# Performance work log

Measured on AMD Instinct MI355X. Metric: run time of the kernel, lower is better.

The kernel has to match this reference:

```python
import jax, jax.numpy as jnp
import numpy as np

N_NODES = 50000
N_EDGES = 800000
D_IN = 128
D_HID = 512
D_OUT = 128


def setup_inputs() -> dict:
    key = jax.random.key(0)
    k1, k2, k3, k4, k5, k6 = jax.random.split(key, 6)
    input_matrix = jax.random.normal(k1, (N_NODES, D_IN), dtype=jnp.float32)
    adjacency_coo_matrix = jax.random.randint(k2, (2, N_EDGES), 0, N_NODES, dtype=jnp.int64)
    # fc net params (torch Linear: y = x @ W.T + b); store W already transposed [D_IN, D_HID]
    lim_fc = 1.0 / np.sqrt(D_IN)
    fc_w = jax.random.uniform(k3, (D_IN, D_HID), dtype=jnp.float32, minval=-lim_fc, maxval=lim_fc)
    fc_b = jax.random.uniform(k4, (D_HID,), dtype=jnp.float32, minval=-lim_fc, maxval=lim_fc)
    # xavier_uniform for [D_IN + D_HID, D_OUT]
    lim_w = np.sqrt(6.0 / (D_IN + D_HID + D_OUT))
    weights_matrix = jax.random.uniform(k5, (D_IN + D_HID, D_OUT), dtype=jnp.float32, minval=-lim_w, maxval=lim_w)
    return {
        "input_matrix": input_matrix,
        "fc_w": fc_w,
        "fc_b": fc_b,
        "weights_matrix": weights_matrix,
        "adjacency_coo_matrix": adjacency_coo_matrix,
    }


def reference(input_matrix, fc_w, fc_b, weights_matrix, adjacency_coo_matrix):
    edge_src, edge_trg = adjacency_coo_matrix[0], adjacency_coo_matrix[1]
    n_nodes = input_matrix.shape[0]
    # gather neighbor features: [E, D_IN]
    neighbors = input_matrix[edge_trg]
    # per-edge MLP + relu: [E, D_HID]
    neighbors_repr = jax.nn.relu(neighbors @ fc_w + fc_b)
    # scatter-max reduce into per-node slots; relu outputs are >= 0, and
    # empty segments map to 0 (matching torch_scatter zero-fill), so clamp at 0
    agg = jax.ops.segment_max(neighbors_repr, edge_src, num_segments=n_nodes)
    agg = jnp.maximum(agg, 0.0)
    concat = jnp.concatenate([input_matrix, agg], axis=1)  # [N, D_IN + D_HID]
    return concat @ weights_matrix  # [N, D_OUT]
```

## Files before the change

kernel.cpp:

```cpp
#include <hip/hip_runtime.h>
#include <hip/hip_bf16.h>

#define N_NODES 50000
#define N_EDGES 800000
#define D_IN 128
#define D_HID 512
#define D_OUT 128
#define CAT_DIM 640
#define CAP 64

typedef __attribute__((ext_vector_type(8))) short short8;
typedef __attribute__((ext_vector_type(4))) float floatx4;

__device__ __forceinline__ unsigned short f2bf(float f) {
    unsigned u = __float_as_uint(f);
    unsigned r = u + 0x7fffu + ((u >> 16) & 1u);
    return (unsigned short)(r >> 16);
}


#define PREP_CASTX_BLOCKS   6250
#define PREP_FCW_BLOCKS      256
#define PREP_W2_BLOCKS       320
#define PREP_DEG_BLOCKS      196
#define PREP_TOTAL_BLOCKS  (PREP_CASTX_BLOCKS + PREP_FCW_BLOCKS + PREP_W2_BLOCKS + PREP_DEG_BLOCKS + 1)

__global__ void prep_kernel(const float* __restrict__ X, const float* __restrict__ fcW,
                            const float* __restrict__ Wm, const int* __restrict__ adj,
                            unsigned short* __restrict__ concat,
                            unsigned short* __restrict__ fcwT,
                            unsigned short* __restrict__ WT,
                            int* __restrict__ deg, int* __restrict__ flag) {
    int b = blockIdx.x;
    int tid = threadIdx.x;
    if (b < PREP_CASTX_BLOCKS) {
        int t = b * 256 + tid;
        int row = t >> 5;
        int cg2 = (t & 31) * 4;
        float4 v = *(const float4*)(X + (size_t)row * D_IN + cg2);
        unsigned short o[4] = { f2bf(v.x), f2bf(v.y), f2bf(v.z), f2bf(v.w) };
        *(unsigned long long*)(concat + (size_t)row * CAT_DIM + cg2) = *(unsigned long long*)o;
        return;
    }
    b -= PREP_CASTX_BLOCKS;
    if (b < PREP_FCW_BLOCKS) {
        int idx = b * 256 + tid;
        int k = idx >> 9;
        int n = idx & (D_HID - 1);
        fcwT[n * D_IN + k] = f2bf(fcW[idx]);
        return;
    }
    b -= PREP_FCW_BLOCKS;
    if (b < PREP_W2_BLOCKS) {
        int idx = b * 256 + tid;
        int k = idx >> 7;
        int n = idx & (D_OUT - 1);
        WT[n * CAT_DIM + k] = f2bf(Wm[idx]);
        return;
    }
    b -= PREP_W2_BLOCKS;
    if (b < PREP_DEG_BLOCKS) {
        int idx = b * 256 + tid;
        if (idx < N_NODES) deg[idx] = 0;
        return;
    }
    if (tid < 64) {
        int v = adj[2 * tid + 1];
        unsigned long long m = __ballot(v != 0);
        if (tid == 0) *flag = (m == 0ULL) ? 2 : 1;
    }
}


__device__ __forceinline__ void hist_edges(const int* __restrict__ adj, int s, int e0,
                                           int* __restrict__ deg, int* __restrict__ edge_list) {
    int src0, src1, trg0, trg1;
    if (s == 2) {
        int4 vs = *(const int4*)(adj + 2 * (size_t)e0);
        int4 vt = *(const int4*)(adj + 2 * ((size_t)N_EDGES + e0));
        src0 = vs.x; src1 = vs.z;
        trg0 = vt.x; trg1 = vt.z;
    } else {
        int2 vs = *(const int2*)(adj + e0);
        int2 vt = *(const int2*)(adj + N_EDGES + e0);
        src0 = vs.x; src1 = vs.y;
        trg0 = vt.x; trg1 = vt.y;
    }
    int p0 = atomicAdd(&deg[src0], 1);
    if (p0 < CAP) edge_list[src0 * CAP + p0] = trg0;
    int p1 = atomicAdd(&deg[src1], 1);
    if (p1 < CAP) edge_list[src1 * CAP + p1] = trg1;
}


#define GPAD 8
#define SM64_BYTES ((64 + 128) * (64 + GPAD) * 2)

template<int BIAS_RELU, int OUT_BF16>
__device__ __forceinline__ void gemm_tile64(char* smem,
    const unsigned short* __restrict__ A, int lda,
    const unsigned short* __restrict__ Bt, int ldb,
    const float* __restrict__ bias, void* __restrict__ Cout, int ldc,
    int M, int K, int bm, int bn)
{
    constexpr int BK = 64;
    typedef unsigned short Row[BK + GPAD];
    Row* As = (Row*)smem;
    Row* Bs = (Row*)(smem + 64 * (BK + GPAD) * 2);
    int tid = threadIdx.x;
    int lane = tid & 63, w = tid >> 6;
    int wm = (w >> 1) * 32, wn = (w & 1) * 64;
    int q = lane >> 4, l16 = lane & 15;
    floatx4 acc[2][4] = {};
    int ra = tid >> 2;
    int ca = (tid & 3) * 8;
    int rb = tid >> 1;
    int cb = (tid & 1) * 8;

    for (int k0 = 0; k0 < K; k0 += BK) {
        {
            int gr = bm + ra;
            const unsigned short* ap = A + (size_t)gr * lda + k0 + ca;
            #pragma unroll
            for (int p = 0; p < 2; ++p) {
                uint4 va = make_uint4(0u, 0u, 0u, 0u);
                if (gr < M) va = *(const uint4*)(ap + p * 32);
                *(uint4*)(&As[ra][ca + p * 32]) = va;
            }
        }
        {
            const unsigned short* bp = Bt + (size_t)(bn + rb) * ldb + k0 + cb;
            #pragma unroll
            for (int p = 0; p < 4; ++p)
                *(uint4*)(&Bs[rb][cb + p * 16]) = *(const uint4*)(bp + p * 16);
        }
        __syncthreads();
        #pragma unroll
        for (int ks = 0; ks < 2; ++ks) {
            short8 af[2], bf[4];
            #pragma unroll
            for (int mi = 0; mi < 2; ++mi)
                af[mi] = *(const short8*)(&As[wm + mi * 16 + l16][ks * 32 + q * 8]);
            #pragma unroll
            for (int ni = 0; ni < 4; ++ni)
                bf[ni] = *(const short8*)(&Bs[wn + ni * 16 + l16][ks * 32 + q * 8]);
            #pragma unroll
            for (int mi = 0; mi < 2; ++mi)
                #pragma unroll
                for (int ni = 0; ni < 4; ++ni)
                    acc[mi][ni] = __builtin_amdgcn_mfma_f32_16x16x32_bf16(af[mi], bf[ni], acc[mi][ni], 0, 0, 0);
        }
        __syncthreads();
    }

    #pragma unroll
    for (int mi = 0; mi < 2; ++mi) {
        #pragma unroll
        for (int ni = 0; ni < 4; ++ni) {
            #pragma unroll
            for (int r = 0; r < 4; ++r) {
                int row = bm + wm + mi * 16 + q * 4 + r;
                int col = bn + wn + ni * 16 + l16;
                if (row < M) {
                    float v = acc[mi][ni][r];
                    if (BIAS_RELU) v = fmaxf(v + bias[col], 0.0f);
                    if (OUT_BF16) ((unsigned short*)Cout)[(size_t)row * ldc + col] = f2bf(v);
                    else          ((float*)Cout)[(size_t)row * ldc + col] = v;
                }
            }
        }
    }
}


#define HIST_VB     1563
#define GEMM1_MT     782
#define GEMM1_TILES (GEMM1_MT * 4)

__global__ __launch_bounds__(256)
void mid_kernel(const int* __restrict__ adj, const int* __restrict__ flag,
                int* __restrict__ deg, int* __restrict__ edge_list,
                const unsigned short* __restrict__ concat,
                const unsigned short* __restrict__ fcwT,
                const float* __restrict__ fcb,
                unsigned short* __restrict__ F) {
    if (blockIdx.x < HIST_VB) {
        int e0 = (blockIdx.x * 256 + threadIdx.x) * 2;
        if (e0 < N_EDGES) hist_edges(adj, flag[0], e0, deg, edge_list);
        return;
    }
    __shared__ char smem[SM64_BYTES];
    int tile = blockIdx.x - HIST_VB;
    gemm_tile64<1, 1>(smem, concat, CAT_DIM, fcwT, D_IN, fcb, F, D_HID,
                      N_NODES, D_IN, (tile >> 2) * 64, (tile & 3) * 128);
}


__device__ __forceinline__ void fmax_bf16x8(float* acc, const uint4& p) {
    const unsigned* a = (const unsigned*)&p;
    #pragma unroll
    for (int j = 0; j < 4; ++j) {
        unsigned u = a[j];
        acc[2 * j]     = fmaxf(acc[2 * j],     __uint_as_float(u << 16));
        acc[2 * j + 1] = fmaxf(acc[2 * j + 1], __uint_as_float(u & 0xffff0000u));
    }
}

__global__ __launch_bounds__(256)
void aggregate_kernel(const unsigned short* __restrict__ F,
                      const int* __restrict__ deg,
                      const int* __restrict__ edge_list,
                      unsigned short* __restrict__ concat) {
    int gw = (blockIdx.x * 256 + threadIdx.x) >> 6;
    if (gw >= N_NODES) return;
    int lane = threadIdx.x & 63;
    int d = deg[gw];
    d = d < CAP ? d : CAP;
    const int* el = edge_list + gw * CAP;
    float acc[8] = {0.f, 0.f, 0.f, 0.f, 0.f, 0.f, 0.f, 0.f};
    int i = 0;
    for (; i + 2 <= d; i += 2) {
        int t0 = el[i], t1 = el[i + 1];
        uint4 p0 = *(const uint4*)(F + (size_t)t0 * D_HID + lane * 8);
        uint4 p1 = *(const uint4*)(F + (size_t)t1 * D_HID + lane * 8);
        fmax_bf16x8(acc, p0);
        fmax_bf16x8(acc, p1);
    }
    if (i < d) {
        uint4 p0 = *(const uint4*)(F + (size_t)el[i] * D_HID + lane * 8);
        fmax_bf16x8(acc, p0);
    }
    unsigned out[4];
    #pragma unroll
    for (int j = 0; j < 4; ++j) {
        unsigned lo = __float_as_uint(acc[2 * j]) >> 16;
        unsigned hi = __float_as_uint(acc[2 * j + 1]) & 0xffff0000u;
        out[j] = lo | hi;
    }
    *(uint4*)(concat + (size_t)gw * CAT_DIM + D_IN + lane * 8) = *(uint4*)out;
}


__global__ __launch_bounds__(256)
void gemm2_kernel(const unsigned short* __restrict__ concat,
                  const unsigned short* __restrict__ WT,
                  float* __restrict__ out) {
    __shared__ char smem[SM64_BYTES];
    gemm_tile64<0, 0>(smem, concat, CAT_DIM, WT, CAT_DIM, nullptr, out, D_OUT,
                      N_NODES, CAT_DIM, blockIdx.x * 64, 0);
}


extern "C" void kernel_launch(void* const* d_in, const int* in_sizes, int n_in,
                              void* d_out, int out_size, void* d_ws, size_t ws_size,
                              hipStream_t stream) {
    const float* X    = (const float*)d_in[0];
    const float* fc_w = (const float*)d_in[1];
    const float* fc_b = (const float*)d_in[2];
    const float* Wm   = (const float*)d_in[3];
    const int*   adj  = (const int*)d_in[4];
    float* outp = (float*)d_out;

    char* ws = (char*)d_ws;
    size_t off = 0;
    auto alloc = [&](size_t bytes) -> void* {
        void* p = ws + off;
        off = (off + bytes + 255) & ~(size_t)255;
        return p;
    };
    unsigned short* concat = (unsigned short*)alloc((size_t)N_NODES * CAT_DIM * 2);
    unsigned short* F      = (unsigned short*)alloc((size_t)N_NODES * D_HID * 2);
    unsigned short* fcwT   = (unsigned short*)alloc((size_t)D_HID * D_IN * 2);
    unsigned short* WT     = (unsigned short*)alloc((size_t)D_OUT * CAT_DIM * 2);
    int* deg       = (int*)alloc((size_t)N_NODES * 4);
    int* edge_list = (int*)alloc((size_t)N_NODES * CAP * 4);
    int* flag      = (int*)alloc(256);

    prep_kernel<<<PREP_TOTAL_BLOCKS, 256, 0, stream>>>(X, fc_w, Wm, adj, concat, fcwT, WT, deg, flag);
    mid_kernel<<<HIST_VB + GEMM1_TILES, 256, 0, stream>>>(adj, flag, deg, edge_list,
                                                          concat, fcwT, fc_b, F);
    aggregate_kernel<<<(N_NODES * 64) / 256, 256, 0, stream>>>(F, deg, edge_list, concat);
    gemm2_kernel<<<GEMM1_MT, 256, 0, stream>>>(concat, WT, outp);
}
```

Baseline: 288.9 us.

## Fuse scatter-max aggregation with the output GEMM, dropping the concat buffer

Merges the aggregation and second GEMM into one kernel. Each block aggregates 32 nodes into shared memory, then runs the output GEMM from shared memory plus a compact bf16 copy of X. The concat buffer and its global write and reread go away, along with one launch. B-operand fragments now load straight from global with no LDS staging, aggregation unrolls by 4, and the smaller 32-row tiles with serial per-wave node loops may reduce parallelism.

```diff
diff --git a/kernel.cpp b/kernel.cpp
--- a/kernel.cpp
+++ b/kernel.cpp
@@ -27,19 +27,17 @@
 
 __global__ void prep_kernel(const float* __restrict__ X, const float* __restrict__ fcW,
                             const float* __restrict__ Wm, const int* __restrict__ adj,
-                            unsigned short* __restrict__ concat,
+                            unsigned short* __restrict__ Xb,
                             unsigned short* __restrict__ fcwT,
                             unsigned short* __restrict__ WT,
                             int* __restrict__ deg, int* __restrict__ flag) {
     int b = blockIdx.x;
     int tid = threadIdx.x;
     if (b < PREP_CASTX_BLOCKS) {
-        int t = b * 256 + tid;
-        int row = t >> 5;
-        int cg2 = (t & 31) * 4;
-        float4 v = *(const float4*)(X + (size_t)row * D_IN + cg2);
+        size_t base = ((size_t)b * 256 + tid) * 4;
+        float4 v = *(const float4*)(X + base);
         unsigned short o[4] = { f2bf(v.x), f2bf(v.y), f2bf(v.z), f2bf(v.w) };
-        *(unsigned long long*)(concat + (size_t)row * CAT_DIM + cg2) = *(unsigned long long*)o;
+        *(unsigned long long*)(Xb + base) = *(unsigned long long*)o;
         return;
     }
     b -= PREP_CASTX_BLOCKS;
@@ -96,12 +94,11 @@
 #define GPAD 8
 #define SM64_BYTES ((64 + 128) * (64 + GPAD) * 2)
 
-template<int BIAS_RELU, int OUT_BF16>
-__device__ __forceinline__ void gemm_tile64(char* smem,
-    const unsigned short* __restrict__ A, int lda,
-    const unsigned short* __restrict__ Bt, int ldb,
-    const float* __restrict__ bias, void* __restrict__ Cout, int ldc,
-    int M, int K, int bm, int bn)
+__device__ __forceinline__ void gemm1_tile(char* smem,
+    const unsigned short* __restrict__ A,
+    const unsigned short* __restrict__ Bt,
+    const float* __restrict__ bias,
+    unsigned short* __restrict__ F, int bm, int bn)
 {
     constexpr int BK = 64;
     typedef unsigned short Row[BK + GPAD];
@@ -117,19 +114,19 @@
     int rb = tid >> 1;
     int cb = (tid & 1) * 8;
 
-    for (int k0 = 0; k0 < K; k0 += BK) {
+    for (int k0 = 0; k0 < D_IN; k0 += BK) {
         {
             int gr = bm + ra;
-            const unsigned short* ap = A + (size_t)gr * lda + k0 + ca;
+            const unsigned short* ap = A + (size_t)gr * D_IN + k0 + ca;
             #pragma unroll
             for (int p = 0; p < 2; ++p) {
                 uint4 va = make_uint4(0u, 0u, 0u, 0u);
-                if (gr < M) va = *(const uint4*)(ap + p * 32);
+                if (gr < N_NODES) va = *(const uint4*)(ap + p * 32);
                 *(uint4*)(&As[ra][ca + p * 32]) = va;
             }
         }
         {
-            const unsigned short* bp = Bt + (size_t)(bn + rb) * ldb + k0 + cb;
+            const unsigned short* bp = Bt + (size_t)(bn + rb) * D_IN + k0 + cb;
             #pragma unroll
             for (int p = 0; p < 4; ++p)
                 *(uint4*)(&Bs[rb][cb + p * 16]) = *(const uint4*)(bp + p * 16);
@@ -161,11 +158,9 @@
             for (int r = 0; r < 4; ++r) {
                 int row = bm + wm + mi * 16 + q * 4 + r;
                 int col = bn + wn + ni * 16 + l16;
-                if (row < M) {
-                    float v = acc[mi][ni][r];
-                    if (BIAS_RELU) v = fmaxf(v + bias[col], 0.0f);
-                    if (OUT_BF16) ((unsigned short*)Cout)[(size_t)row * ldc + col] = f2bf(v);
-                    else          ((float*)Cout)[(size_t)row * ldc + col] = v;
+                if (row < N_NODES) {
+                    float v = fmaxf(acc[mi][ni][r] + bias[col], 0.0f);
+                    F[(size_t)row * D_HID + col] = f2bf(v);
                 }
             }
         }
@@ -180,7 +175,7 @@
 __global__ __launch_bounds__(256)
 void mid_kernel(const int* __restrict__ adj, const int* __restrict__ flag,
                 int* __restrict__ deg, int* __restrict__ edge_list,
-                const unsigned short* __restrict__ concat,
+                const unsigned short* __restrict__ Xb,
                 const unsigned short* __restrict__ fcwT,
                 const float* __restrict__ fcb,
                 unsigned short* __restrict__ F) {
@@ -191,10 +186,13 @@
     }
     __shared__ char smem[SM64_BYTES];
     int tile = blockIdx.x - HIST_VB;
-    gemm_tile64<1, 1>(smem, concat, CAT_DIM, fcwT, D_IN, fcb, F, D_HID,
-                      N_NODES, D_IN, (tile >> 2) * 64, (tile & 3) * 128);
-}
-
+    gemm1_tile(smem, Xb, fcwT, fcb, F, (tile >> 2) * 64, (tile & 3) * 128);
+}
+
+
+#define AG_BM     32
+#define AG_BLOCKS 1563
+#define APAD      8
 
 __device__ __forceinline__ void fmax_bf16x8(float* acc, const uint4& p) {
     const unsigned* a = (const unsigned*)&p;
@@ -207,47 +205,86 @@
 }
 
 __global__ __launch_bounds__(256)
-void aggregate_kernel(const unsigned short* __restrict__ F,
-                      const int* __restrict__ deg,
-                      const int* __restrict__ edge_list,
-                      unsigned short* __restrict__ concat) {
-    int gw = (blockIdx.x * 256 + threadIdx.x) >> 6;
-    if (gw >= N_NODES) return;
-    int lane = threadIdx.x & 63;
-    int d = deg[gw];
-    d = d < CAP ? d : CAP;
-    const int* el = edge_list + gw * CAP;
-    float acc[8] = {0.f, 0.f, 0.f, 0.f, 0.f, 0.f, 0.f, 0.f};
-    int i = 0;
-    for (; i + 2 <= d; i += 2) {
-        int t0 = el[i], t1 = el[i + 1];
-        uint4 p0 = *(const uint4*)(F + (size_t)t0 * D_HID + lane * 8);
-        uint4 p1 = *(const uint4*)(F + (size_t)t1 * D_HID + lane * 8);
-        fmax_bf16x8(acc, p0);
-        fmax_bf16x8(acc, p1);
-    }
-    if (i < d) {
-        uint4 p0 = *(const uint4*)(F + (size_t)el[i] * D_HID + lane * 8);
-        fmax_bf16x8(acc, p0);
-    }
-    unsigned out[4];
-    #pragma unroll
-    for (int j = 0; j < 4; ++j) {
-        unsigned lo = __float_as_uint(acc[2 * j]) >> 16;
-        unsigned hi = __float_as_uint(acc[2 * j + 1]) & 0xffff0000u;
-        out[j] = lo | hi;
-    }
-    *(uint4*)(concat + (size_t)gw * CAT_DIM + D_IN + lane * 8) = *(uint4*)out;
-}
-
-
-__global__ __launch_bounds__(256)
-void gemm2_kernel(const unsigned short* __restrict__ concat,
-                  const unsigned short* __restrict__ WT,
-                  float* __restrict__ out) {
-    __shared__ char smem[SM64_BYTES];
-    gemm_tile64<0, 0>(smem, concat, CAT_DIM, WT, CAT_DIM, nullptr, out, D_OUT,
-                      N_NODES, CAT_DIM, blockIdx.x * 64, 0);
+void aggemm_kernel(const unsigned short* __restrict__ F,
+                   const int* __restrict__ deg,
+                   const int* __restrict__ edge_list,
+                   const unsigned short* __restrict__ Xb,
+                   const unsigned short* __restrict__ WT,
+                   float* __restrict__ out) {
+    __shared__ unsigned short aggS[AG_BM][D_HID + APAD];
+    int tid = threadIdx.x;
+    int lane = tid & 63, wv = tid >> 6;
+    int bm = blockIdx.x * AG_BM;
+
+    for (int nn = 0; nn < 8; ++nn) {
+        int lr = wv * 8 + nn;
+        int node = bm + lr;
+        if (node < N_NODES) {
+            int d = deg[node];
+            d = d < CAP ? d : CAP;
+            const int* el = edge_list + node * CAP;
+            float acc[8] = {0.f, 0.f, 0.f, 0.f, 0.f, 0.f, 0.f, 0.f};
+            int i = 0;
+            for (; i + 4 <= d; i += 4) {
+                uint4 p0 = *(const uint4*)(F + (size_t)el[i]     * D_HID + lane * 8);
+                uint4 p1 = *(const uint4*)(F + (size_t)el[i + 1] * D_HID + lane * 8);
+                uint4 p2 = *(const uint4*)(F + (size_t)el[i + 2] * D_HID + lane * 8);
+                uint4 p3 = *(const uint4*)(F + (size_t)el[i + 3] * D_HID + lane * 8);
+                fmax_bf16x8(acc, p0);
+                fmax_bf16x8(acc, p1);
+                fmax_bf16x8(acc, p2);
+                fmax_bf16x8(acc, p3);
+            }
+            for (; i < d; ++i) {
+                uint4 p0 = *(const uint4*)(F + (size_t)el[i] * D_HID + lane * 8);
+                fmax_bf16x8(acc, p0);
+            }
+            unsigned o[4];
+            #pragma unroll
+            for (int j = 0; j < 4; ++j) {
+                unsigned lo = __float_as_uint(acc[2 * j]) >> 16;
+                unsigned hi = __float_as_uint(acc[2 * j + 1]) & 0xffff0000u;
+                o[j] = lo | hi;
+            }
+            *(uint4*)(&aggS[lr][lane * 8]) = *(uint4*)o;
+        }
+    }
+    __syncthreads();
+
+    int wm = (wv >> 1) * 16, wn = (wv & 1) * 64;
+    int q = lane >> 4, l16 = lane & 15;
+    floatx4 acc[4] = {};
+    int arow = bm + wm + l16;
+
+    #pragma unroll
+    for (int k0 = 0; k0 < D_IN; k0 += 32) {
+        short8 af = {};
+        if (arow < N_NODES) af = *(const short8*)(Xb + (size_t)arow * D_IN + k0 + q * 8);
+        #pragma unroll
+        for (int ni = 0; ni < 4; ++ni) {
+            short8 bf = *(const short8*)(WT + (size_t)(wn + ni * 16 + l16) * CAT_DIM + k0 + q * 8);
+            acc[ni] = __builtin_amdgcn_mfma_f32_16x16x32_bf16(af, bf, acc[ni], 0, 0, 0);
+        }
+    }
+    #pragma unroll
+    for (int k0 = 0; k0 < D_HID; k0 += 32) {
+        short8 af = *(const short8*)(&aggS[wm + l16][k0 + q * 8]);
+        #pragma unroll
+        for (int ni = 0; ni < 4; ++ni) {
+            short8 bf = *(const short8*)(WT + (size_t)(wn + ni * 16 + l16) * CAT_DIM + D_IN + k0 + q * 8);
+            acc[ni] = __builtin_amdgcn_mfma_f32_16x16x32_bf16(af, bf, acc[ni], 0, 0, 0);
+        }
+    }
+
+    #pragma unroll
+    for (int ni = 0; ni < 4; ++ni) {
+        #pragma unroll
+        for (int r = 0; r < 4; ++r) {
+            int row = bm + wm + q * 4 + r;
+            if (row < N_NODES)
+                out[(size_t)row * D_OUT + wn + ni * 16 + l16] = acc[ni][r];
+        }
+    }
 }
 
 
@@ -268,17 +305,16 @@
         off = (off + bytes + 255) & ~(size_t)255;
         return p;
     };
-    unsigned short* concat = (unsigned short*)alloc((size_t)N_NODES * CAT_DIM * 2);
-    unsigned short* F      = (unsigned short*)alloc((size_t)N_NODES * D_HID * 2);
-    unsigned short* fcwT   = (unsigned short*)alloc((size_t)D_HID * D_IN * 2);
-    unsigned short* WT     = (unsigned short*)alloc((size_t)D_OUT * CAT_DIM * 2);
+    unsigned short* Xb   = (unsigned short*)alloc((size_t)N_NODES * D_IN * 2);
+    unsigned short* F    = (unsigned short*)alloc((size_t)N_NODES * D_HID * 2);
+    unsigned short* fcwT = (unsigned short*)alloc((size_t)D_HID * D_IN * 2);
+    unsigned short* WT   = (unsigned short*)alloc((size_t)D_OUT * CAT_DIM * 2);
     int* deg       = (int*)alloc((size_t)N_NODES * 4);
     int* edge_list = (int*)alloc((size_t)N_NODES * CAP * 4);
     int* flag      = (int*)alloc(256);
 
-    prep_kernel<<<PREP_TOTAL_BLOCKS, 256, 0, stream>>>(X, fc_w, Wm, adj, concat, fcwT, WT, deg, flag);
+    prep_kernel<<<PREP_TOTAL_BLOCKS, 256, 0, stream>>>(X, fc_w, Wm, adj, Xb, fcwT, WT, deg, flag);
     mid_kernel<<<HIST_VB + GEMM1_TILES, 256, 0, stream>>>(adj, flag, deg, edge_list,
-                                                          concat, fcwT, fc_b, F);
-    aggregate_kernel<<<(N_NODES * 64) / 256, 256, 0, stream>>>(F, deg, edge_list, concat);
-    gemm2_kernel<<<GEMM1_MT, 256, 0, stream>>>(concat, WT, outp);
-}
+                                                          Xb, fcwT, fc_b, F);
+    aggemm_kernel<<<AG_BLOCKS, 256, 0, stream>>>(F, deg, edge_list, Xb, WT, outp);
+}
```

New measurement: 321.4 us. +11.3%, slower.

## Fuse X bf16 cast into GEMMs and reuse A tile across N tiles

Applied to the files above, without the earlier changes.

Removes the separate X-to-bf16 cast pass and the concat buffer. Both GEMMs now read fp32 X directly and convert it while loading into shared memory. GEMM1 now loads a 64-row A tile once and loops over four 128-column N tiles, so the grid is 782 blocks instead of 3128. Aggregate writes into a separate A2 buffer, and GEMM2 walks K in five 128-wide chunks. This saves a full read and write of X in bf16 and the repeated A loads, at the cost of fewer and longer GEMM1 blocks and reading X in fp32 twice.

```diff
diff --git a/kernel.cpp b/kernel.cpp
--- a/kernel.cpp
+++ b/kernel.cpp
@@ -19,47 +19,35 @@
 }
 
 
-#define PREP_CASTX_BLOCKS   6250
-#define PREP_FCW_BLOCKS      256
-#define PREP_W2_BLOCKS       320
-#define PREP_DEG_BLOCKS      196
-#define PREP_TOTAL_BLOCKS  (PREP_CASTX_BLOCKS + PREP_FCW_BLOCKS + PREP_W2_BLOCKS + PREP_DEG_BLOCKS + 1)
-
-__global__ void prep_kernel(const float* __restrict__ X, const float* __restrict__ fcW,
-                            const float* __restrict__ Wm, const int* __restrict__ adj,
-                            unsigned short* __restrict__ concat,
+#define PS_FCW_BLOCKS 256
+#define PS_W2_BLOCKS  320
+#define PS_DEG_BLOCKS 196
+#define PS_TOTAL (PS_FCW_BLOCKS + PS_W2_BLOCKS + PS_DEG_BLOCKS + 1)
+
+__global__ void prep_kernel(const float* __restrict__ fcW, const float* __restrict__ Wm,
+                            const int* __restrict__ adj,
                             unsigned short* __restrict__ fcwT,
                             unsigned short* __restrict__ WT,
                             int* __restrict__ deg, int* __restrict__ flag) {
     int b = blockIdx.x;
     int tid = threadIdx.x;
-    if (b < PREP_CASTX_BLOCKS) {
-        int t = b * 256 + tid;
-        int row = t >> 5;
-        int cg2 = (t & 31) * 4;
-        float4 v = *(const float4*)(X + (size_t)row * D_IN + cg2);
-        unsigned short o[4] = { f2bf(v.x), f2bf(v.y), f2bf(v.z), f2bf(v.w) };
-        *(unsigned long long*)(concat + (size_t)row * CAT_DIM + cg2) = *(unsigned long long*)o;
-        return;
-    }
-    b -= PREP_CASTX_BLOCKS;
-    if (b < PREP_FCW_BLOCKS) {
+    if (b < PS_FCW_BLOCKS) {
         int idx = b * 256 + tid;
         int k = idx >> 9;
         int n = idx & (D_HID - 1);
         fcwT[n * D_IN + k] = f2bf(fcW[idx]);
         return;
     }
-    b -= PREP_FCW_BLOCKS;
-    if (b < PREP_W2_BLOCKS) {
+    b -= PS_FCW_BLOCKS;
+    if (b < PS_W2_BLOCKS) {
         int idx = b * 256 + tid;
         int k = idx >> 7;
         int n = idx & (D_OUT - 1);
         WT[n * CAT_DIM + k] = f2bf(Wm[idx]);
         return;
     }
-    b -= PREP_W2_BLOCKS;
-    if (b < PREP_DEG_BLOCKS) {
+    b -= PS_W2_BLOCKS;
+    if (b < PS_DEG_BLOCKS) {
         int idx = b * 256 + tid;
         if (idx < N_NODES) deg[idx] = 0;
         return;
@@ -93,94 +81,14 @@
 }
 
 
-#define GPAD 8
-#define SM64_BYTES ((64 + 128) * (64 + GPAD) * 2)
-
-template<int BIAS_RELU, int OUT_BF16>
-__device__ __forceinline__ void gemm_tile64(char* smem,
-    const unsigned short* __restrict__ A, int lda,
-    const unsigned short* __restrict__ Bt, int ldb,
-    const float* __restrict__ bias, void* __restrict__ Cout, int ldc,
-    int M, int K, int bm, int bn)
-{
-    constexpr int BK = 64;
-    typedef unsigned short Row[BK + GPAD];
-    Row* As = (Row*)smem;
-    Row* Bs = (Row*)(smem + 64 * (BK + GPAD) * 2);
-    int tid = threadIdx.x;
-    int lane = tid & 63, w = tid >> 6;
-    int wm = (w >> 1) * 32, wn = (w & 1) * 64;
-    int q = lane >> 4, l16 = lane & 15;
-    floatx4 acc[2][4] = {};
-    int ra = tid >> 2;
-    int ca = (tid & 3) * 8;
-    int rb = tid >> 1;
-    int cb = (tid & 1) * 8;
-
-    for (int k0 = 0; k0 < K; k0 += BK) {
-        {
-            int gr = bm + ra;
-            const unsigned short* ap = A + (size_t)gr * lda + k0 + ca;
-            #pragma unroll
-            for (int p = 0; p < 2; ++p) {
-                uint4 va = make_uint4(0u, 0u, 0u, 0u);
-                if (gr < M) va = *(const uint4*)(ap + p * 32);
-                *(uint4*)(&As[ra][ca + p * 32]) = va;
-            }
-        }
-        {
-            const unsigned short* bp = Bt + (size_t)(bn + rb) * ldb + k0 + cb;
-            #pragma unroll
-            for (int p = 0; p < 4; ++p)
-                *(uint4*)(&Bs[rb][cb + p * 16]) = *(const uint4*)(bp + p * 16);
-        }
-        __syncthreads();
-        #pragma unroll
-        for (int ks = 0; ks < 2; ++ks) {
-            short8 af[2], bf[4];
-            #pragma unroll
-            for (int mi = 0; mi < 2; ++mi)
-                af[mi] = *(const short8*)(&As[wm + mi * 16 + l16][ks * 32 + q * 8]);
-            #pragma unroll
-            for (int ni = 0; ni < 4; ++ni)
-                bf[ni] = *(const short8*)(&Bs[wn + ni * 16 + l16][ks * 32 + q * 8]);
-            #pragma unroll
-            for (int mi = 0; mi < 2; ++mi)
-                #pragma unroll
-                for (int ni = 0; ni < 4; ++ni)
-                    acc[mi][ni] = __builtin_amdgcn_mfma_f32_16x16x32_bf16(af[mi], bf[ni], acc[mi][ni], 0, 0, 0);
-        }
-        __syncthreads();
-    }
-
-    #pragma unroll
-    for (int mi = 0; mi < 2; ++mi) {
-        #pragma unroll
-        for (int ni = 0; ni < 4; ++ni) {
-            #pragma unroll
-            for (int r = 0; r < 4; ++r) {
-                int row = bm + wm + mi * 16 + q * 4 + r;
-                int col = bn + wn + ni * 16 + l16;
-                if (row < M) {
-                    float v = acc[mi][ni][r];
-                    if (BIAS_RELU) v = fmaxf(v + bias[col], 0.0f);
-                    if (OUT_BF16) ((unsigned short*)Cout)[(size_t)row * ldc + col] = f2bf(v);
-                    else          ((float*)Cout)[(size_t)row * ldc + col] = v;
-                }
-            }
-        }
-    }
-}
-
-
-#define HIST_VB     1563
-#define GEMM1_MT     782
-#define GEMM1_TILES (GEMM1_MT * 4)
+#define HIST_VB   1563
+#define GEMM1_MT   782
+#define LPAD 8
 
 __global__ __launch_bounds__(256)
 void mid_kernel(const int* __restrict__ adj, const int* __restrict__ flag,
                 int* __restrict__ deg, int* __restrict__ edge_list,
-                const unsigned short* __restrict__ concat,
+                const float* __restrict__ X,
                 const unsigned short* __restrict__ fcwT,
                 const float* __restrict__ fcb,
                 unsigned short* __restrict__ F) {
@@ -189,10 +97,72 @@
         if (e0 < N_EDGES) hist_edges(adj, flag[0], e0, deg, edge_list);
         return;
     }
-    __shared__ char smem[SM64_BYTES];
-    int tile = blockIdx.x - HIST_VB;
-    gemm_tile64<1, 1>(smem, concat, CAT_DIM, fcwT, D_IN, fcb, F, D_HID,
-                      N_NODES, D_IN, (tile >> 2) * 64, (tile & 3) * 128);
+    __shared__ unsigned short As[64][D_IN + LPAD];
+    __shared__ unsigned short Bs[128][D_IN + LPAD];
+    int tid = threadIdx.x;
+    int lane = tid & 63, w = tid >> 6;
+    int wm = (w >> 1) * 32, wn = (w & 1) * 64;
+    int q = lane >> 4, l16 = lane & 15;
+    int bm = (blockIdx.x - HIST_VB) * 64;
+
+    {
+        int ra = tid >> 2;
+        int ca = (tid & 3) * 32;
+        int gr = bm + ra;
+        #pragma unroll
+        for (int p = 0; p < 8; ++p) {
+            float4 v = make_float4(0.f, 0.f, 0.f, 0.f);
+            if (gr < N_NODES) v = *(const float4*)(X + (size_t)gr * D_IN + ca + p * 4);
+            unsigned short o[4] = { f2bf(v.x), f2bf(v.y), f2bf(v.z), f2bf(v.w) };
+            *(unsigned long long*)(&As[ra][ca + p * 4]) = *(unsigned long long*)o;
+        }
+    }
+
+    int rb = tid >> 1;
+    int cb = (tid & 1) * 64;
+    for (int nt = 0; nt < 4; ++nt) {
+        if (nt) __syncthreads();
+        {
+            const unsigned short* bp = fcwT + (size_t)(nt * 128 + rb) * D_IN + cb;
+            #pragma unroll
+            for (int p = 0; p < 8; ++p)
+                *(uint4*)(&Bs[rb][cb + p * 8]) = *(const uint4*)(bp + p * 8);
+        }
+        __syncthreads();
+
+        floatx4 acc[2][4] = {};
+        #pragma unroll
+        for (int ks = 0; ks < 4; ++ks) {
+            short8 af[2], bf[4];
+            #pragma unroll
+            for (int mi = 0; mi < 2; ++mi)
+                af[mi] = *(const short8*)(&As[wm + mi * 16 + l16][ks * 32 + q * 8]);
+            #pragma unroll
+            for (int ni = 0; ni < 4; ++ni)
+                bf[ni] = *(const short8*)(&Bs[wn + ni * 16 + l16][ks * 32 + q * 8]);
+            #pragma unroll
+            for (int mi = 0; mi < 2; ++mi)
+                #pragma unroll
+                for (int ni = 0; ni < 4; ++ni)
+                    acc[mi][ni] = __builtin_amdgcn_mfma_f32_16x16x32_bf16(af[mi], bf[ni], acc[mi][ni], 0, 0, 0);
+        }
+
+        #pragma unroll
+        for (int mi = 0; mi < 2; ++mi) {
+            #pragma unroll
+            for (int ni = 0; ni < 4; ++ni) {
+                #pragma unroll
+                for (int r = 0; r < 4; ++r) {
+                    int row = bm + wm + mi * 16 + q * 4 + r;
+                    int col = nt * 128 + wn + ni * 16 + l16;
+                    if (row < N_NODES) {
+                        float v = fmaxf(acc[mi][ni][r] + fcb[col], 0.0f);
+                        F[(size_t)row * D_HID + col] = f2bf(v);
+                    }
+                }
+            }
+        }
+    }
 }
 
 
@@ -210,7 +180,7 @@
 void aggregate_kernel(const unsigned short* __restrict__ F,
                       const int* __restrict__ deg,
                       const int* __restrict__ edge_list,
-                      unsigned short* __restrict__ concat) {
+                      unsigned short* __restrict__ A2) {
     int gw = (blockIdx.x * 256 + threadIdx.x) >> 6;
     if (gw >= N_NODES) return;
     int lane = threadIdx.x & 63;
@@ -237,17 +207,88 @@
         unsigned hi = __float_as_uint(acc[2 * j + 1]) & 0xffff0000u;
         out[j] = lo | hi;
     }
-    *(uint4*)(concat + (size_t)gw * CAT_DIM + D_IN + lane * 8) = *(uint4*)out;
+    *(uint4*)(A2 + (size_t)gw * D_HID + lane * 8) = *(uint4*)out;
 }
 
 
 __global__ __launch_bounds__(256)
-void gemm2_kernel(const unsigned short* __restrict__ concat,
+void gemm2_kernel(const float* __restrict__ X,
+                  const unsigned short* __restrict__ A2,
                   const unsigned short* __restrict__ WT,
                   float* __restrict__ out) {
-    __shared__ char smem[SM64_BYTES];
-    gemm_tile64<0, 0>(smem, concat, CAT_DIM, WT, CAT_DIM, nullptr, out, D_OUT,
-                      N_NODES, CAT_DIM, blockIdx.x * 64, 0);
+    __shared__ unsigned short As[64][128 + LPAD];
+    __shared__ unsigned short Bs[128][128 + LPAD];
+    int tid = threadIdx.x;
+    int lane = tid & 63, w = tid >> 6;
+    int wm = (w >> 1) * 32, wn = (w & 1) * 64;
+    int q = lane >> 4, l16 = lane & 15;
+    int bm = blockIdx.x * 64;
+
+    floatx4 acc[2][4] = {};
+    int ra = tid >> 2;
+    int ca = (tid & 3) * 32;
+    int rb = tid >> 1;
+    int cb = (tid & 1) * 64;
+
+    #pragma unroll
+    for (int it = 0; it < 5; ++it) {
+        if (it) __syncthreads();
+        int gr = bm + ra;
+        if (it == 0) {
+            #pragma unroll
+            for (int p = 0; p < 8; ++p) {
+                float4 v = make_float4(0.f, 0.f, 0.f, 0.f);
+                if (gr < N_NODES) v = *(const float4*)(X + (size_t)gr * D_IN + ca + p * 4);
+                unsigned short o[4] = { f2bf(v.x), f2bf(v.y), f2bf(v.z), f2bf(v.w) };
+                *(unsigned long long*)(&As[ra][ca + p * 4]) = *(unsigned long long*)o;
+            }
+        } else {
+            const unsigned short* ap = A2 + (size_t)gr * D_HID + (it - 1) * 128 + ca;
+            #pragma unroll
+            for (int p = 0; p < 4; ++p) {
+                uint4 v = make_uint4(0u, 0u, 0u, 0u);
+                if (gr < N_NODES) v = *(const uint4*)(ap + p * 8);
+                *(uint4*)(&As[ra][ca + p * 8]) = v;
+            }
+        }
+        {
+            const unsigned short* bp = WT + (size_t)rb * CAT_DIM + it * 128 + cb;
+            #pragma unroll
+            for (int p = 0; p < 8; ++p)
+                *(uint4*)(&Bs[rb][cb + p * 8]) = *(const uint4*)(bp + p * 8);
+        }
+        __syncthreads();
+
+        #pragma unroll
+        for (int ks = 0; ks < 4; ++ks) {
+            short8 af[2], bf[4];
+            #pragma unroll
+            for (int mi = 0; mi < 2; ++mi)
+                af[mi] = *(const short8*)(&As[wm + mi * 16 + l16][ks * 32 + q * 8]);
+            #pragma unroll
+            for (int ni = 0; ni < 4; ++ni)
+                bf[ni] = *(const short8*)(&Bs[wn + ni * 16 + l16][ks * 32 + q * 8]);
+            #pragma unroll
+            for (int mi = 0; mi < 2; ++mi)
+                #pragma unroll
+                for (int ni = 0; ni < 4; ++ni)
+                    acc[mi][ni] = __builtin_amdgcn_mfma_f32_16x16x32_bf16(af[mi], bf[ni], acc[mi][ni], 0, 0, 0);
+        }
+    }
+
+    #pragma unroll
+    for (int mi = 0; mi < 2; ++mi) {
+        #pragma unroll
+        for (int ni = 0; ni < 4; ++ni) {
+            #pragma unroll
+            for (int r = 0; r < 4; ++r) {
+                int row = bm + wm + mi * 16 + q * 4 + r;
+                int col = wn + ni * 16 + l16;
+                if (row < N_NODES)
+                    out[(size_t)row * D_OUT + col] = acc[mi][ni][r];
+            }
+        }
+    }
 }
 
 
@@ -268,17 +309,17 @@
         off = (off + bytes + 255) & ~(size_t)255;
         return p;
     };
-    unsigned short* concat = (unsigned short*)alloc((size_t)N_NODES * CAT_DIM * 2);
-    unsigned short* F      = (unsigned short*)alloc((size_t)N_NODES * D_HID * 2);
-    unsigned short* fcwT   = (unsigned short*)alloc((size_t)D_HID * D_IN * 2);
-    unsigned short* WT     = (unsigned short*)alloc((size_t)D_OUT * CAT_DIM * 2);
+    unsigned short* F    = (unsigned short*)alloc((size_t)N_NODES * D_HID * 2);
+    unsigned short* A2   = (unsigned short*)alloc((size_t)N_NODES * D_HID * 2);
+    unsigned short* fcwT = (unsigned short*)alloc((size_t)D_HID * D_IN * 2);
+    unsigned short* WT   = (unsigned short*)alloc((size_t)D_OUT * CAT_DIM * 2);
     int* deg       = (int*)alloc((size_t)N_NODES * 4);
     int* edge_list = (int*)alloc((size_t)N_NODES * CAP * 4);
     int* flag      = (int*)alloc(256);
 
-    prep_kernel<<<PREP_TOTAL_BLOCKS, 256, 0, stream>>>(X, fc_w, Wm, adj, concat, fcwT, WT, deg, flag);
-    mid_kernel<<<HIST_VB + GEMM1_TILES, 256, 0, stream>>>(adj, flag, deg, edge_list,
-                                                          concat, fcwT, fc_b, F);
-    aggregate_kernel<<<(N_NODES * 64) / 256, 256, 0, stream>>>(F, deg, edge_list, concat);
-    gemm2_kernel<<<GEMM1_MT, 256, 0, stream>>>(concat, WT, outp);
-}
+    prep_kernel<<<PS_TOTAL, 256, 0, stream>>>(fc_w, Wm, adj, fcwT, WT, deg, flag);
+    mid_kernel<<<HIST_VB + GEMM1_MT, 256, 0, stream>>>(adj, flag, deg, edge_list,
+                                                       X, fcwT, fc_b, F);
+    aggregate_kernel<<<(N_NODES * 64) / 256, 256, 0, stream>>>(F, deg, edge_list, A2);
+    gemm2_kernel<<<GEMM1_MT, 256, 0, stream>>>(X, A2, WT, outp);
+}
```

Result: slower. 338.2 us (+17.1%).

## Drop LDS staging in GEMMs and split GEMM2 K to overlap with aggregation

Applied to the files above, without the earlier changes.

The shared-memory-staged GEMM tile is replaced with a version that loads MFMA fragments straight from global memory, which removes the syncthreads barriers and LDS traffic. GEMM2 is split along K: the X part (first 128 columns) runs inside the aggregation kernel as extra blocks, and a later kernel accumulates the aggregated part into the output with read-modify-write. The degree array is now zeroed with hipMemsetAsync rather than by dedicated prep blocks. In exchange there are uncoalesced, repeated global loads with no LDS reuse, an extra read-modify-write of the fp32 output, and one more launch for the memset.

```diff
diff --git a/kernel.cpp b/kernel.cpp
--- a/kernel.cpp
+++ b/kernel.cpp
@@ -22,15 +22,14 @@
 #define PREP_CASTX_BLOCKS   6250
 #define PREP_FCW_BLOCKS      256
 #define PREP_W2_BLOCKS       320
-#define PREP_DEG_BLOCKS      196
-#define PREP_TOTAL_BLOCKS  (PREP_CASTX_BLOCKS + PREP_FCW_BLOCKS + PREP_W2_BLOCKS + PREP_DEG_BLOCKS + 1)
+#define PREP_TOTAL (PREP_CASTX_BLOCKS + PREP_FCW_BLOCKS + PREP_W2_BLOCKS + 1)
 
 __global__ void prep_kernel(const float* __restrict__ X, const float* __restrict__ fcW,
                             const float* __restrict__ Wm, const int* __restrict__ adj,
                             unsigned short* __restrict__ concat,
                             unsigned short* __restrict__ fcwT,
                             unsigned short* __restrict__ WT,
-                            int* __restrict__ deg, int* __restrict__ flag) {
+                            int* __restrict__ flag) {
     int b = blockIdx.x;
     int tid = threadIdx.x;
     if (b < PREP_CASTX_BLOCKS) {
@@ -56,12 +55,6 @@
         int k = idx >> 7;
         int n = idx & (D_OUT - 1);
         WT[n * CAT_DIM + k] = f2bf(Wm[idx]);
-        return;
-    }
-    b -= PREP_W2_BLOCKS;
-    if (b < PREP_DEG_BLOCKS) {
-        int idx = b * 256 + tid;
-        if (idx < N_NODES) deg[idx] = 0;
         return;
     }
     if (tid < 64) {
@@ -93,64 +86,44 @@
 }
 
 
-#define GPAD 8
-#define SM64_BYTES ((64 + 128) * (64 + GPAD) * 2)
-
-template<int BIAS_RELU, int OUT_BF16>
-__device__ __forceinline__ void gemm_tile64(char* smem,
+template<int BIAS_RELU, int OUT_MODE>
+__device__ __forceinline__ void mfma_tile_nolds(
     const unsigned short* __restrict__ A, int lda,
     const unsigned short* __restrict__ Bt, int ldb,
-    const float* __restrict__ bias, void* __restrict__ Cout, int ldc,
-    int M, int K, int bm, int bn)
+    const float* __restrict__ bias, void* __restrict__ C, int ldc,
+    int M, int k_lo, int k_hi, int bm, int bn)
 {
-    constexpr int BK = 64;
-    typedef unsigned short Row[BK + GPAD];
-    Row* As = (Row*)smem;
-    Row* Bs = (Row*)(smem + 64 * (BK + GPAD) * 2);
     int tid = threadIdx.x;
     int lane = tid & 63, w = tid >> 6;
     int wm = (w >> 1) * 32, wn = (w & 1) * 64;
     int q = lane >> 4, l16 = lane & 15;
     floatx4 acc[2][4] = {};
-    int ra = tid >> 2;
-    int ca = (tid & 3) * 8;
-    int rb = tid >> 1;
-    int cb = (tid & 1) * 8;
-
-    for (int k0 = 0; k0 < K; k0 += BK) {
-        {
-            int gr = bm + ra;
-            const unsigned short* ap = A + (size_t)gr * lda + k0 + ca;
-            #pragma unroll
-            for (int p = 0; p < 2; ++p) {
-                uint4 va = make_uint4(0u, 0u, 0u, 0u);
-                if (gr < M) va = *(const uint4*)(ap + p * 32);
-                *(uint4*)(&As[ra][ca + p * 32]) = va;
-            }
+
+    int arow0 = bm + wm + l16;
+    int arow1 = arow0 + 16;
+    bool v0 = arow0 < M, v1 = arow1 < M;
+    const unsigned short* a0 = A + (size_t)arow0 * lda + q * 8;
+    const unsigned short* a1 = A + (size_t)arow1 * lda + q * 8;
+    const unsigned short* bp0 = Bt + (size_t)(bn + wn + l16) * ldb + q * 8;
+    const unsigned short* bp1 = bp0 + (size_t)16 * ldb;
+    const unsigned short* bp2 = bp0 + (size_t)32 * ldb;
+    const unsigned short* bp3 = bp0 + (size_t)48 * ldb;
+
+    #pragma unroll 4
+    for (int k0 = k_lo; k0 < k_hi; k0 += 32) {
+        short8 af0 = {}, af1 = {};
+        if (v0) af0 = *(const short8*)(a0 + k0);
+        if (v1) af1 = *(const short8*)(a1 + k0);
+        short8 bf[4];
+        bf[0] = *(const short8*)(bp0 + k0);
+        bf[1] = *(const short8*)(bp1 + k0);
+        bf[2] = *(const short8*)(bp2 + k0);
+        bf[3] = *(const short8*)(bp3 + k0);
+        #pragma unroll
+        for (int ni = 0; ni < 4; ++ni) {
+            acc[0][ni] = __builtin_amdgcn_mfma_f32_16x16x32_bf16(af0, bf[ni], acc[0][ni], 0, 0, 0);
+            acc[1][ni] = __builtin_amdgcn_mfma_f32_16x16x32_bf16(af1, bf[ni], acc[1][ni], 0, 0, 0);
         }
-        {
-            const unsigned short* bp = Bt + (size_t)(bn + rb) * ldb + k0 + cb;
-            #pragma unroll
-            for (int p = 0; p < 4; ++p)
-                *(uint4*)(&Bs[rb][cb + p * 16]) = *(const uint4*)(bp + p * 16);
-        }
-        __syncthreads();
-        #pragma unroll
-        for (int ks = 0; ks < 2; ++ks) {
-            short8 af[2], bf[4];
-            #pragma unroll
-            for (int mi = 0; mi < 2; ++mi)
-                af[mi] = *(const short8*)(&As[wm + mi * 16 + l16][ks * 32 + q * 8]);
-            #pragma unroll
-            for (int ni = 0; ni < 4; ++ni)
-                bf[ni] = *(const short8*)(&Bs[wn + ni * 16 + l16][ks * 32 + q * 8]);
-            #pragma unroll
-            for (int mi = 0; mi < 2; ++mi)
-                #pragma unroll
-                for (int ni = 0; ni < 4; ++ni)
-                    acc[mi][ni] = __builtin_amdgcn_mfma_f32_16x16x32_bf16(af[mi], bf[ni], acc[mi][ni], 0, 0, 0);
-        }
-        __syncthreads();
     }
 
     #pragma unroll
@@ -164,8 +137,14 @@
                 if (row < M) {
                     float v = acc[mi][ni][r];
                     if (BIAS_RELU) v = fmaxf(v + bias[col], 0.0f);
-                    if (OUT_BF16) ((unsigned short*)Cout)[(size_t)row * ldc + col] = f2bf(v);
-                    else          ((float*)Cout)[(size_t)row * ldc + col] = v;
+                    if (OUT_MODE == 0)
+                        ((float*)C)[(size_t)row * ldc + col] = v;
+                    else if (OUT_MODE == 1)
+                        ((unsigned short*)C)[(size_t)row * ldc + col] = f2bf(v);
+                    else {
+                        float* o = (float*)C + (size_t)row * ldc + col;
+                        *o = *o + v;
+                    }
                 }
             }
         }
@@ -173,8 +152,8 @@
 }
 
 
-#define HIST_VB     1563
-#define GEMM1_MT     782
+#define HIST_VB   1563
+#define GEMM1_MT   782
 #define GEMM1_TILES (GEMM1_MT * 4)
 
 __global__ __launch_bounds__(256)
@@ -189,12 +168,13 @@
         if (e0 < N_EDGES) hist_edges(adj, flag[0], e0, deg, edge_list);
         return;
     }
-    __shared__ char smem[SM64_BYTES];
     int tile = blockIdx.x - HIST_VB;
-    gemm_tile64<1, 1>(smem, concat, CAT_DIM, fcwT, D_IN, fcb, F, D_HID,
-                      N_NODES, D_IN, (tile >> 2) * 64, (tile & 3) * 128);
-}
-
+    mfma_tile_nolds<1, 1>(concat, CAT_DIM, fcwT, D_IN, fcb, F, D_HID,
+                          N_NODES, 0, D_IN, (tile >> 2) * 64, (tile & 3) * 128);
+}
+
+
+#define GEMM2A_VB 782
 
 __device__ __forceinline__ void fmax_bf16x8(float* acc, const uint4& p) {
     const unsigned* a = (const unsigned*)&p;
@@ -207,11 +187,18 @@
 }
 
 __global__ __launch_bounds__(256)
-void aggregate_kernel(const unsigned short* __restrict__ F,
-                      const int* __restrict__ deg,
-                      const int* __restrict__ edge_list,
-                      unsigned short* __restrict__ concat) {
-    int gw = (blockIdx.x * 256 + threadIdx.x) >> 6;
+void aggmix_kernel(const unsigned short* __restrict__ F,
+                   const int* __restrict__ deg,
+                   const int* __restrict__ edge_list,
+                   unsigned short* __restrict__ concat,
+                   const unsigned short* __restrict__ WT,
+                   float* __restrict__ out) {
+    if (blockIdx.x < GEMM2A_VB) {
+        mfma_tile_nolds<0, 0>(concat, CAT_DIM, WT, CAT_DIM, nullptr, out, D_OUT,
+                              N_NODES, 0, D_IN, blockIdx.x * 64, 0);
+        return;
+    }
+    int gw = (blockIdx.x - GEMM2A_VB) * 4 + (threadIdx.x >> 6);
     if (gw >= N_NODES) return;
     int lane = threadIdx.x & 63;
     int d = deg[gw];
@@ -230,24 +217,23 @@
         uint4 p0 = *(const uint4*)(F + (size_t)el[i] * D_HID + lane * 8);
         fmax_bf16x8(acc, p0);
     }
-    unsigned out[4];
+    unsigned o[4];
     #pragma unroll
     for (int j = 0; j < 4; ++j) {
         unsigned lo = __float_as_uint(acc[2 * j]) >> 16;
         unsigned hi = __float_as_uint(acc[2 * j + 1]) & 0xffff0000u;
-        out[j] = lo | hi;
-    }
-    *(uint4*)(concat + (size_t)gw * CAT_DIM + D_IN + lane * 8) = *(uint4*)out;
+        o[j] = lo | hi;
+    }
+    *(uint4*)(concat + (size_t)gw * CAT_DIM + D_IN + lane * 8) = *(uint4*)o;
 }
 
 
 __global__ __launch_bounds__(256)
-void gemm2_kernel(const unsigned short* __restrict__ concat,
-                  const unsigned short* __restrict__ WT,
-                  float* __restrict__ out) {
-    __shared__ char smem[SM64_BYTES];
-    gemm_tile64<0, 0>(smem, concat, CAT_DIM, WT, CAT_DIM, nullptr, out, D_OUT,
-                      N_NODES, CAT_DIM, blockIdx.x * 64, 0);
+void gemm2b_kernel(const unsigned short* __restrict__ concat,
+                   const unsigned short* __restrict__ WT,
+                   float* __restrict__ out) {
+    mfma_tile_nolds<0, 2>(concat, CAT_DIM, WT, CAT_DIM, nullptr, out, D_OUT,
+                          N_NODES, D_IN, CAT_DIM, blockIdx.x * 64, 0);
 }
 
 
@@ -276,9 +262,11 @@
     int* edge_list = (int*)alloc((size_t)N_NODES * CAP * 4);
     int* flag      = (int*)alloc(256);
 
-    prep_kernel<<<PREP_TOTAL_BLOCKS, 256, 0, stream>>>(X, fc_w, Wm, adj, concat, fcwT, WT, deg, flag);
+    hipMemsetAsync(deg, 0, (size_t)N_NODES * 4, stream);
+    prep_kernel<<<PREP_TOTAL, 256, 0, stream>>>(X, fc_w, Wm, adj, concat, fcwT, WT, flag);
     mid_kernel<<<HIST_VB + GEMM1_TILES, 256, 0, stream>>>(adj, flag, deg, edge_list,
                                                           concat, fcwT, fc_b, F);
-    aggregate_kernel<<<(N_NODES * 64) / 256, 256, 0, stream>>>(F, deg, edge_list, concat);
-    gemm2_kernel<<<GEMM1_MT, 256, 0, stream>>>(concat, WT, outp);
-}
+    aggmix_kernel<<<GEMM2A_VB + (N_NODES / 4), 256, 0, stream>>>(F, deg, edge_list,
+                                                                 concat, WT, outp);
+    gemm2b_kernel<<<GEMM1_MT, 256, 0, stream>>>(concat, WT, outp);
+}
```

Result: slower. 358.3 us (+24.0%).
